# Optimization experiments

Hardware: AMD Instinct MI355X
Metric: run time of the kernel (lower is better)

Reference implementation:

```python
import jax, jax.numpy as jnp
import numpy as np

B, NQ, NK = 16, 1024, 1024
DQ = DK = DV = 512
H = 4
DH = DV // H  # 128


def layer_norm(x, g, b, eps=1e-5):
    mu = jnp.mean(x, axis=-1, keepdims=True)
    var = jnp.var(x, axis=-1, keepdims=True)  # biased, matches torch LayerNorm
    return (x - mu) / jnp.sqrt(var + eps) * g + b


def setup_inputs() -> dict:
    key = jax.random.key(0)
    ks = jax.random.split(key, 16)
    s = lambda d: 1.0 / np.sqrt(d)
    return {
        "Q": jax.random.normal(ks[0], (B, NQ, DQ), jnp.float32),
        "K": jax.random.normal(ks[1], (B, NK, DK), jnp.float32),
        "weights": jax.random.uniform(ks[2], (H * B, NQ, NK), jnp.float32),
        "Wq": jax.random.normal(ks[3], (DV, DQ), jnp.float32) * s(DQ),
        "bq": jnp.zeros((DV,), jnp.float32),
        "Wk": jax.random.normal(ks[4], (DV, DK), jnp.float32) * s(DK),
        "bk": jnp.zeros((DV,), jnp.float32),
        "Wv": jax.random.normal(ks[5], (DV, DK), jnp.float32) * s(DK),
        "bv": jnp.zeros((DV,), jnp.float32),
        "Wo": jax.random.normal(ks[6], (DV, DV), jnp.float32) * s(DV),
        "bo": jnp.zeros((DV,), jnp.float32),
        "g0": jnp.ones((DV,), jnp.float32),
        "beta0": jnp.zeros((DV,), jnp.float32),
        "g1": jnp.ones((DV,), jnp.float32),
        "beta1": jnp.zeros((DV,), jnp.float32),
    }


def reference(Q, K, weights, Wq, bq, Wk, bk, Wv, bv, Wo, bo, g0, beta0, g1, beta1):
    q = Q @ Wq.T + bq  # [B,NQ,DV]
    k = K @ Wk.T + bk  # [B,NK,DV]
    v = K @ Wv.T + bv  # [B,NK,DV]

    # torch split(dh, 2) + cat(0) == head-major [H,B,N,DH]
    def heads(x, n):
        return x.reshape(B, n, H, DH).transpose(2, 0, 1, 3)

    q_, k_, v_ = heads(q, NQ), heads(k, NK), heads(v, NK)

    # NOTE: original scales by sqrt(dim_V), not sqrt(head_dim)
    scores = jnp.einsum("hbqd,hbkd->hbqk", q_, k_) / np.sqrt(DV)
    log_w = jnp.log(jnp.clip(weights, 0.0, None)).reshape(H, B, NQ, NK)
    A = jax.nn.softmax(scores + log_w, axis=-1)  # [H,B,NQ,NK]

    o = q_ + jnp.einsum("hbqk,hbkd->hbqd", A, v_)  # residual inside heads
    # split(B,0)+cat(2) == merge heads back to [B,NQ,DV]
    O = o.transpose(1, 2, 0, 3).reshape(B, NQ, DV)
    O = layer_norm(O, g0, beta0)
    O = O + jax.nn.relu(O @ Wo.T + bo)
    O = layer_norm(O, g1, beta1)
    return O
```

## Files before the change

kernel.cpp:

```cpp
#include <hip/hip_runtime.h>

typedef unsigned short u16;
typedef unsigned int u32;
typedef __attribute__((ext_vector_type(8))) short short8;
typedef __attribute__((ext_vector_type(4))) float f32x4;
typedef __attribute__((ext_vector_type(2))) u32 uintx2;
typedef __attribute__((address_space(3))) u32 lds32;
typedef const __attribute__((address_space(1))) u32 g32c;

__device__ __forceinline__ u16 f2bf(float f) {
  union { float f; u32 u; } v; v.f = f;
  return (u16)((v.u + 0x7fffu + ((v.u >> 16) & 1u)) >> 16);
}
__device__ __forceinline__ float bf2f(u16 h) {
  union { u32 u; float f; } v; v.u = ((u32)h) << 16;
  return v.f;
}

__global__ void cvt_w_kernel(const float* __restrict__ Wq, const float* __restrict__ Wk,
                             const float* __restrict__ Wv, const float* __restrict__ Wo,
                             u16* __restrict__ dst) {
  int m = blockIdx.y;
  const float* s = (m == 0) ? Wq : (m == 1) ? Wk : (m == 2) ? Wv : Wo;
  int idx = (blockIdx.x * 256 + threadIdx.x) * 4;
  float4 v = *(const float4*)(s + idx);
  uintx2 pk;
  pk[0] = (u32)f2bf(v.x) | ((u32)f2bf(v.y) << 16);
  pk[1] = (u32)f2bf(v.z) | ((u32)f2bf(v.w) << 16);
  *(uintx2*)(dst + m * 262144 + idx) = pk;
}

template <bool AF32, bool OUTMODE, bool TRANSV>
__device__ __forceinline__ void gemm_bt_body(const void* __restrict__ Ap,
                                             const u16* __restrict__ Bw,
                                             const float* __restrict__ bias,
                                             u16* __restrict__ C) {
  __shared__ u16 ldsA[128 * 64];
  __shared__ u16 ldsB[128 * 64];
  const int t = threadIdx.x;
  const int lane = t & 63, wid = t >> 6;
  const int lr = lane & 15, lg = lane >> 4;
  const int n0 = blockIdx.x * 128;
  const int m0 = blockIdx.y * 128;
  const int wr = (wid >> 1) * 64, wc = (wid & 1) * 64;

  f32x4 acc[4][4];
#pragma unroll
  for (int i = 0; i < 4; ++i)
#pragma unroll
    for (int j = 0; j < 4; ++j)
#pragma unroll
      for (int r = 0; r < 4; ++r) acc[i][j][r] = 0.f;

  for (int kt = 0; kt < 512; kt += 64) {
    __syncthreads();
#pragma unroll
    for (int i = 0; i < 4; ++i) {
      int lin = i * 256 + t;
      int row = lin >> 3, u = lin & 7;
      int pu = u ^ (row & 7);
      if constexpr (AF32) {
        const float* src = (const float*)Ap + (size_t)(m0 + row) * 512 + kt + u * 8;
        float4 v0 = *(const float4*)src;
        float4 v1 = *(const float4*)(src + 4);
        short8 pk;
        pk[0] = (short)f2bf(v0.x); pk[1] = (short)f2bf(v0.y);
        pk[2] = (short)f2bf(v0.z); pk[3] = (short)f2bf(v0.w);
        pk[4] = (short)f2bf(v1.x); pk[5] = (short)f2bf(v1.y);
        pk[6] = (short)f2bf(v1.z); pk[7] = (short)f2bf(v1.w);
        *(short8*)&ldsA[row * 64 + pu * 8] = pk;
      } else {
        const u16* src = (const u16*)Ap + (size_t)(m0 + row) * 512 + kt + u * 8;
        *(short8*)&ldsA[row * 64 + pu * 8] = *(const short8*)src;
      }
      const u16* bsrc = Bw + (size_t)(n0 + row) * 512 + kt + u * 8;
      *(short8*)&ldsB[row * 64 + pu * 8] = *(const short8*)bsrc;
    }
    __syncthreads();
#pragma unroll
    for (int kk = 0; kk < 2; ++kk) {
      short8 af[4], bfr[4];
#pragma unroll
      for (int mf = 0; mf < 4; ++mf) {
        int row = wr + mf * 16 + lr;
        af[mf] = *(const short8*)&ldsA[row * 64 + (((kk * 4 + lg) ^ (row & 7)) * 8)];
      }
#pragma unroll
      for (int nf = 0; nf < 4; ++nf) {
        int row = wc + nf * 16 + lr;
        bfr[nf] = *(const short8*)&ldsB[row * 64 + (((kk * 4 + lg) ^ (row & 7)) * 8)];
      }
#pragma unroll
      for (int mf = 0; mf < 4; ++mf)
#pragma unroll
        for (int nf = 0; nf < 4; ++nf)
          acc[mf][nf] =
              __builtin_amdgcn_mfma_f32_16x16x32_bf16(af[mf], bfr[nf], acc[mf][nf], 0, 0, 0);
    }
  }

  if constexpr (TRANSV) {
    const int h_ = n0 >> 7;
#pragma unroll
    for (int mf = 0; mf < 4; ++mf)
#pragma unroll
      for (int nf = 0; nf < 4; ++nf) {
        int d = wc + nf * 16 + lr;
        int rr0 = m0 + wr + mf * 16 + lg * 4;
        int b_ = rr0 >> 10;
        int k0 = rr0 & 1023;
        float bvv = bias[n0 + d];
        uintx2 pk;
        pk[0] = (u32)f2bf(acc[mf][nf][0] + bvv) | ((u32)f2bf(acc[mf][nf][1] + bvv) << 16);
        pk[1] = (u32)f2bf(acc[mf][nf][2] + bvv) | ((u32)f2bf(acc[mf][nf][3] + bvv) << 16);
        *(uintx2*)(C + (((size_t)b_ * 4 + h_) * 128 + d) * 1024 + k0) = pk;
      }
  } else {
#pragma unroll
    for (int mf = 0; mf < 4; ++mf)
#pragma unroll
      for (int nf = 0; nf < 4; ++nf) {
        int c = n0 + wc + nf * 16 + lr;
        float bv = bias[c];
#pragma unroll
        for (int r = 0; r < 4; ++r) {
          int rr = m0 + wr + mf * 16 + lg * 4 + r;
          float v = acc[mf][nf][r] + bv;
          if constexpr (OUTMODE) {
            v = v > 0.f ? v : 0.f;
            v += bf2f(((const u16*)Ap)[(size_t)rr * 512 + c]);
          }
          C[(size_t)rr * 512 + c] = f2bf(v);
        }
      }
  }
}

__global__ __launch_bounds__(256) void gemm3_kernel(const float* __restrict__ Q,
                                                    const float* __restrict__ K,
                                                    const u16* __restrict__ Wb,
                                                    const float* __restrict__ bq,
                                                    const float* __restrict__ bk,
                                                    const float* __restrict__ bv,
                                                    u16* qb, u16* kb, u16* vbT) {
  int z = blockIdx.z;
  if (z == 2) {
    gemm_bt_body<true, false, true>(K, Wb + 524288, bv, vbT);
  } else {
    const void* Ap = (z == 0) ? (const void*)Q : (const void*)K;
    const u16* Bw = Wb + z * 262144;
    const float* bias = (z == 0) ? bq : bk;
    u16* C = (z == 0) ? qb : kb;
    gemm_bt_body<true, false, false>(Ap, Bw, bias, C);
  }
}

__global__ __launch_bounds__(256) void gemmo_kernel(const u16* __restrict__ X,
                                                    const u16* __restrict__ Wb,
                                                    const float* __restrict__ bo,
                                                    u16* Z) {
  gemm_bt_body<false, true, false>(X, Wb, bo, Z);
}

__global__ __launch_bounds__(256) void attn_kernel(const u16* __restrict__ qb,
                                                   const u16* __restrict__ kb,
                                                   const u16* __restrict__ vbT,
                                                   const float* __restrict__ Wt,
                                                   u16* __restrict__ Ob) {
  __shared__ __align__(16) u16 ldsK[2][64 * 128];
  __shared__ __align__(16) u16 ldsVT[2][128 * 64];
  __shared__ __align__(16) u16 ldsP[128 * 64];
  const int t = threadIdx.x;
  const int lane = t & 63, wid = t >> 6;
  const int lr = lane & 15, lg = lane >> 4;
  const int bid = blockIdx.x;
  const int x_ = bid & 7, s_ = bid >> 3;
  const int hb = ((s_ & 7) << 3) | x_;
  const int q0 = (s_ >> 3) * 128;
  const int b = hb & 15;
  const int h = hb >> 4;
  const int wq = wid * 32;
  const size_t kvbase = ((size_t)b * 1024) * 512 + h * 128;
  const size_t vtbase = ((size_t)b * 4 + h) * 131072;
  const float SCALE = 0.044194173824159216f;

  const u16* ksrc[4];
  const u16* vtsrc[4];
#pragma unroll
  for (int i = 0; i < 4; ++i) {
    {
      int lin = i * 256 + t;
      int row = lin >> 4, u = lin & 15;
      ksrc[i] = kb + kvbase + (size_t)row * 512 + ((u ^ (row & 15)) * 8);
    }
    {
      int lin = i * 256 + t;
      int row = lin >> 3, u = lin & 7;
      vtsrc[i] = vbT + vtbase + (size_t)row * 1024 + ((u ^ (row & 7)) * 8);
    }
  }
  const int wslot = (t & 192) * 8;

#define STAGE(bu)                                                                           \
  do {                                                                                      \
    _Pragma("unroll") for (int i_ = 0; i_ < 4; ++i_) {                                      \
      __builtin_amdgcn_global_load_lds((g32c*)(ksrc[i_]),                                   \
                                       (lds32*)(&ldsK[bu][i_ * 2048 + wslot]), 16, 0, 0);   \
      __builtin_amdgcn_global_load_lds((g32c*)(vtsrc[i_]),                                  \
                                       (lds32*)(&ldsVT[bu][i_ * 2048 + wslot]), 16, 0, 0);  \
      ksrc[i_] += 32768;                                                \
      vtsrc[i_] += 64;                                                  \
    }                                                                                       \
  } while (0)

  const float* wp0 = Wt + ((size_t)hb * 1024 + q0 + wq + lr) * 1024 + lg * 4;
  const float* wp1 = wp0 + 16 * 1024;

#define WLOADP(W)                                          \
  do {                                                     \
    _Pragma("unroll") for (int j_ = 0; j_ < 4; ++j_) {     \
      W[j_]     = *(const f32x4*)(wp0 + j_ * 16);          \
      W[4 + j_] = *(const f32x4*)(wp1 + j_ * 16);          \
    }                                                      \
    wp0 += 64; wp1 += 64;                                  \
  } while (0)

  short8 qfr[2][4];
#pragma unroll
  for (int nf = 0; nf < 2; ++nf) {
    const u16* qp = qb + kvbase + (size_t)(q0 + wq + nf * 16 + lr) * 512 + lg * 8;
#pragma unroll
    for (int ds = 0; ds < 4; ++ds) qfr[nf][ds] = *(const short8*)(qp + ds * 32);
  }

  f32x4 oacc[2][8];
#pragma unroll
  for (int i = 0; i < 2; ++i)
#pragma unroll
    for (int j = 0; j < 8; ++j)
#pragma unroll
      for (int r = 0; r < 4; ++r) oacc[i][j][r] = 0.f;
  float lacc[2] = {0.f, 0.f};

  auto tile_compute = [&](const u16* bK, const u16* bVT, const f32x4 (&W)[8]) {
    f32x4 sacc[4][2];
#pragma unroll
    for (int i = 0; i < 4; ++i)
#pragma unroll
      for (int j = 0; j < 2; ++j)
#pragma unroll
        for (int r = 0; r < 4; ++r) sacc[i][j][r] = 0.f;

#pragma unroll
    for (int ds = 0; ds < 4; ++ds) {
      short8 kf[4];
#pragma unroll
      for (int mf = 0; mf < 4; ++mf) {
        int row = mf * 16 + lr;
        kf[mf] = *(const short8*)&bK[row * 128 + (((ds * 4 + lg) ^ (row & 15)) * 8)];
      }
      __builtin_amdgcn_s_setprio(1);
#pragma unroll
      for (int mf = 0; mf < 4; ++mf)
#pragma unroll
        for (int nf = 0; nf < 2; ++nf)
          sacc[mf][nf] =
              __builtin_amdgcn_mfma_f32_16x16x32_bf16(kf[mf], qfr[nf][ds], sacc[mf][nf], 0, 0, 0);
      __builtin_amdgcn_s_setprio(0);
    }

#pragma unroll
    for (int nf = 0; nf < 2; ++nf) {
      int prow = wq + nf * 16 + lr;
#pragma unroll
      for (int mf = 0; mf < 4; ++mf) {
        f32x4 w4 = W[nf * 4 + mf];
        float p0 = w4[0] * __expf(sacc[mf][nf][0] * SCALE);
        float p1 = w4[1] * __expf(sacc[mf][nf][1] * SCALE);
        float p2 = w4[2] * __expf(sacc[mf][nf][2] * SCALE);
        float p3 = w4[3] * __expf(sacc[mf][nf][3] * SCALE);
        lacc[nf] += (p0 + p1) + (p2 + p3);
        uintx2 pk;
        pk[0] = (u32)f2bf(p0) | ((u32)f2bf(p1) << 16);
        pk[1] = (u32)f2bf(p2) | ((u32)f2bf(p3) << 16);
        int byteoff = (prow * 128 + (mf * 16 + lg * 4) * 2) ^ ((prow & 7) << 4);
        *(uintx2*)((char*)ldsP + byteoff) = pk;
      }
    }

#pragma unroll
    for (int ks = 0; ks < 2; ++ks) {
      short8 pa[2];
#pragma unroll
      for (int qf = 0; qf < 2; ++qf) {
        int row = wq + qf * 16 + lr;
        int byteoff = (row * 128 + (ks * 4 + lg) * 16) ^ ((row & 7) << 4);
        pa[qf] = *(const short8*)((const char*)ldsP + byteoff);
      }
      short8 vf[8];
#pragma unroll
      for (int nf = 0; nf < 8; ++nf) {
        int row = nf * 16 + lr;
        vf[nf] = *(const short8*)&bVT[row * 64 + (((ks * 4 + lg) ^ (row & 7)) * 8)];
      }
      __builtin_amdgcn_s_setprio(1);
#pragma unroll
      for (int qf = 0; qf < 2; ++qf)
#pragma unroll
        for (int nf = 0; nf < 8; ++nf)
          oacc[qf][nf] =
              __builtin_amdgcn_mfma_f32_16x16x32_bf16(pa[qf], vf[nf], oacc[qf][nf], 0, 0, 0);
      __builtin_amdgcn_s_setprio(0);
    }
  };

#define SCHED_FENCE() __builtin_amdgcn_sched_barrier(0)
#define WAITBAR(N)                                                 \
  do {                                                             \
    SCHED_FENCE();                                                 \
    asm volatile("s_waitcnt vmcnt(" #N ")" ::: "memory");          \
    __builtin_amdgcn_s_barrier();                                  \
    SCHED_FENCE();                                                 \
  } while (0)
#define BAR()                                                      \
  do {                                                             \
    SCHED_FENCE();                                                 \
    __builtin_amdgcn_s_barrier();                                  \
    SCHED_FENCE();                                                 \
  } while (0)

  f32x4 wA[8], wB[8];
  WLOADP(wA);
  STAGE(0);

  for (int it = 0; it < 8; ++it) {
    {
      STAGE(1);
      WLOADP(wB);
      WAITBAR(16);
      tile_compute(&ldsK[0][0], &ldsVT[0][0], wA);
      BAR();
    }
    {
      if (it < 7) {
        STAGE(0);
        WLOADP(wA);
        WAITBAR(16);
      } else {
        WAITBAR(0);
      }
      tile_compute(&ldsK[1][0], &ldsVT[1][0], wB);
      if (it < 7) BAR();
    }
  }

  float lred[2];
#pragma unroll
  for (int nf = 0; nf < 2; ++nf) {
    float s = lacc[nf];
    s += __shfl_xor(s, 16);
    s += __shfl_xor(s, 32);
    lred[nf] = s;
  }

#pragma unroll
  for (int qf = 0; qf < 2; ++qf)
#pragma unroll
    for (int r = 0; r < 4; ++r) {
      float lv = __shfl(lred[qf], (lane & 48) | (lg * 4 + r));
      float linv = 1.0f / lv;
      int qrow = q0 + wq + qf * 16 + lg * 4 + r;
      size_t base = kvbase + (size_t)qrow * 512;
#pragma unroll
      for (int nf = 0; nf < 8; ++nf) {
        size_t idx = base + nf * 16 + lr;
        Ob[idx] = f2bf(bf2f(qb[idx]) + oacc[qf][nf][r] * linv);
      }
    }
#undef STAGE
#undef WLOADP
#undef WAITBAR
#undef BAR
#undef SCHED_FENCE
}

template <bool F32OUT>
__global__ __launch_bounds__(256) void ln_kernel(const u16* __restrict__ in,
                                                 const float* __restrict__ g,
                                                 const float* __restrict__ be,
                                                 void* __restrict__ outp) {
  const int lane = threadIdx.x & 63, wid = threadIdx.x >> 6;
  const int row = blockIdx.x * 4 + wid;
  const u16* p = in + (size_t)row * 512 + lane * 8;
  short8 v = *(const short8*)p;
  float x[8];
  float s = 0.f, s2 = 0.f;
#pragma unroll
  for (int j = 0; j < 8; ++j) {
    x[j] = bf2f((u16)v[j]);
    s += x[j];
    s2 += x[j] * x[j];
  }
#pragma unroll
  for (int off = 1; off < 64; off <<= 1) {
    s += __shfl_xor(s, off);
    s2 += __shfl_xor(s2, off);
  }
  float mu = s * (1.f / 512.f);
  float var = s2 * (1.f / 512.f) - mu * mu;
  float rs = rsqrtf(var + 1e-5f);
  float4 ga = *(const float4*)(g + lane * 8);
  float4 gb = *(const float4*)(g + lane * 8 + 4);
  float4 ba = *(const float4*)(be + lane * 8);
  float4 bb = *(const float4*)(be + lane * 8 + 4);
  float gg[8] = {ga.x, ga.y, ga.z, ga.w, gb.x, gb.y, gb.z, gb.w};
  float bv[8] = {ba.x, ba.y, ba.z, ba.w, bb.x, bb.y, bb.z, bb.w};
  if constexpr (F32OUT) {
    float* out = (float*)outp + (size_t)row * 512 + lane * 8;
    float4 o0, o1;
    o0.x = (x[0] - mu) * rs * gg[0] + bv[0];
    o0.y = (x[1] - mu) * rs * gg[1] + bv[1];
    o0.z = (x[2] - mu) * rs * gg[2] + bv[2];
    o0.w = (x[3] - mu) * rs * gg[3] + bv[3];
    o1.x = (x[4] - mu) * rs * gg[4] + bv[4];
    o1.y = (x[5] - mu) * rs * gg[5] + bv[5];
    o1.z = (x[6] - mu) * rs * gg[6] + bv[6];
    o1.w = (x[7] - mu) * rs * gg[7] + bv[7];
    *(float4*)out = o0;
    *(float4*)(out + 4) = o1;
  } else {
    short8 o;
#pragma unroll
    for (int j = 0; j < 8; ++j) o[j] = (short)f2bf((x[j] - mu) * rs * gg[j] + bv[j]);
    *(short8*)((u16*)outp + (size_t)row * 512 + lane * 8) = o;
  }
}

extern "C" void kernel_launch(void* const* d_in, const int* in_sizes, int n_in,
                              void* d_out, int out_size, void* d_ws, size_t ws_size,
                              hipStream_t stream) {
  (void)in_sizes; (void)n_in; (void)out_size; (void)ws_size;
  const float* Q   = (const float*)d_in[0];
  const float* K   = (const float*)d_in[1];
  const float* Wt  = (const float*)d_in[2];
  const float* Wq  = (const float*)d_in[3];
  const float* bq  = (const float*)d_in[4];
  const float* Wk  = (const float*)d_in[5];
  const float* bk  = (const float*)d_in[6];
  const float* Wv  = (const float*)d_in[7];
  const float* bv  = (const float*)d_in[8];
  const float* Wo  = (const float*)d_in[9];
  const float* bo  = (const float*)d_in[10];
  const float* g0  = (const float*)d_in[11];
  const float* be0 = (const float*)d_in[12];
  const float* g1  = (const float*)d_in[13];
  const float* be1 = (const float*)d_in[14];

  char* ws = (char*)d_ws;
  const size_t MB16 = 16777216;
  u16* qb  = (u16*)(ws);
  u16* kb  = (u16*)(ws + MB16);
  u16* vbT = (u16*)(ws + 2 * MB16);
  u16* Wb  = (u16*)(ws + 3 * MB16);
  u16* Ob  = (u16*)d_out;

  cvt_w_kernel<<<dim3(256, 4), 256, 0, stream>>>(Wq, Wk, Wv, Wo, Wb);
  gemm3_kernel<<<dim3(4, 128, 3), 256, 0, stream>>>(Q, K, Wb, bq, bk, bv, qb, kb, vbT);
  attn_kernel<<<dim3(512), 256, 0, stream>>>(qb, kb, vbT, Wt, Ob);
  ln_kernel<false><<<4096, 256, 0, stream>>>(Ob, g0, be0, qb);
  gemmo_kernel<<<dim3(4, 128), 256, 0, stream>>>(qb, Wb + 786432, bo, kb);
  ln_kernel<true><<<4096, 256, 0, stream>>>(kb, g1, be1, d_out);
}
```

Baseline: 251.9 us.

## Double-buffer projection GEMMs with async global-to-LDS loads and register prefetch

Rewrites the QKV projection and output GEMMs to use double-buffered LDS tiles. The weight (and bf16 activation) tiles are loaded with direct global-to-LDS loads, and the fp32 A operand is prefetched two stages ahead in registers before conversion to bf16. This overlaps global memory latency with the MFMA work and needs one barrier per k-step instead of two. The cost is double the LDS footprint and more registers, which may lower occupancy.

```diff
diff --git a/kernel.cpp b/kernel.cpp
--- a/kernel.cpp
+++ b/kernel.cpp
@@ -30,19 +30,58 @@
   *(uintx2*)(dst + m * 262144 + idx) = pk;
 }
 
-template <bool AF32, bool OUTMODE, bool TRANSV>
-__device__ __forceinline__ void gemm_bt_body(const void* __restrict__ Ap,
-                                             const u16* __restrict__ Bw,
-                                             const float* __restrict__ bias,
-                                             u16* __restrict__ C) {
-  __shared__ u16 ldsA[128 * 64];
-  __shared__ u16 ldsB[128 * 64];
+
+__device__ __forceinline__ void gemm_tile_mfma(const u16* bA, const u16* bB, int wr, int wc,
+                                               int lr, int lg, f32x4 (&acc)[4][4]) {
+#pragma unroll
+  for (int kk = 0; kk < 2; ++kk) {
+    short8 af[4], bfr[4];
+#pragma unroll
+    for (int mf = 0; mf < 4; ++mf) {
+      int row = wr + mf * 16 + lr;
+      af[mf] = *(const short8*)&bA[row * 64 + (((kk * 4 + lg) ^ (row & 7)) * 8)];
+    }
+#pragma unroll
+    for (int nf = 0; nf < 4; ++nf) {
+      int row = wc + nf * 16 + lr;
+      bfr[nf] = *(const short8*)&bB[row * 64 + (((kk * 4 + lg) ^ (row & 7)) * 8)];
+    }
+#pragma unroll
+    for (int mf = 0; mf < 4; ++mf)
+#pragma unroll
+      for (int nf = 0; nf < 4; ++nf)
+        acc[mf][nf] =
+            __builtin_amdgcn_mfma_f32_16x16x32_bf16(af[mf], bfr[nf], acc[mf][nf], 0, 0, 0);
+  }
+}
+
+template <bool TRANSV>
+__device__ __forceinline__ void gemm_f32a_body(const float* __restrict__ Ap,
+                                               const u16* __restrict__ Bw,
+                                               const float* __restrict__ bias,
+                                               u16* __restrict__ C) {
+  __shared__ __align__(16) u16 ldsA[2][128 * 64];
+  __shared__ __align__(16) u16 ldsB[2][128 * 64];
   const int t = threadIdx.x;
   const int lane = t & 63, wid = t >> 6;
   const int lr = lane & 15, lg = lane >> 4;
   const int n0 = blockIdx.x * 128;
   const int m0 = blockIdx.y * 128;
   const int wr = (wid >> 1) * 64, wc = (wid & 1) * 64;
+  const int wslot = (t & 192) * 8;
+
+  int arow[4], apu[4];
+  const u16* bsrc[4];
+  const float* asrc[4];
+#pragma unroll
+  for (int i = 0; i < 4; ++i) {
+    int lin = i * 256 + t;
+    int row = lin >> 3, u = lin & 7;
+    arow[i] = row;
+    apu[i] = u ^ (row & 7);
+    asrc[i] = Ap + (size_t)(m0 + row) * 512 + u * 8;
+    bsrc[i] = Bw + (size_t)(n0 + row) * 512 + ((u ^ (row & 7)) * 8);
+  }
 
   f32x4 acc[4][4];
 #pragma unroll
@@ -52,52 +91,61 @@
 #pragma unroll
       for (int r = 0; r < 4; ++r) acc[i][j][r] = 0.f;
 
-  for (int kt = 0; kt < 512; kt += 64) {
-    __syncthreads();
-#pragma unroll
-    for (int i = 0; i < 4; ++i) {
-      int lin = i * 256 + t;
-      int row = lin >> 3, u = lin & 7;
-      int pu = u ^ (row & 7);
-      if constexpr (AF32) {
-        const float* src = (const float*)Ap + (size_t)(m0 + row) * 512 + kt + u * 8;
-        float4 v0 = *(const float4*)src;
-        float4 v1 = *(const float4*)(src + 4);
-        short8 pk;
-        pk[0] = (short)f2bf(v0.x); pk[1] = (short)f2bf(v0.y);
-        pk[2] = (short)f2bf(v0.z); pk[3] = (short)f2bf(v0.w);
-        pk[4] = (short)f2bf(v1.x); pk[5] = (short)f2bf(v1.y);
-        pk[6] = (short)f2bf(v1.z); pk[7] = (short)f2bf(v1.w);
-        *(short8*)&ldsA[row * 64 + pu * 8] = pk;
-      } else {
-        const u16* src = (const u16*)Ap + (size_t)(m0 + row) * 512 + kt + u * 8;
-        *(short8*)&ldsA[row * 64 + pu * 8] = *(const short8*)src;
-      }
-      const u16* bsrc = Bw + (size_t)(n0 + row) * 512 + kt + u * 8;
-      *(short8*)&ldsB[row * 64 + pu * 8] = *(const short8*)bsrc;
-    }
-    __syncthreads();
-#pragma unroll
-    for (int kk = 0; kk < 2; ++kk) {
-      short8 af[4], bfr[4];
-#pragma unroll
-      for (int mf = 0; mf < 4; ++mf) {
-        int row = wr + mf * 16 + lr;
-        af[mf] = *(const short8*)&ldsA[row * 64 + (((kk * 4 + lg) ^ (row & 7)) * 8)];
-      }
-#pragma unroll
-      for (int nf = 0; nf < 4; ++nf) {
-        int row = wc + nf * 16 + lr;
-        bfr[nf] = *(const short8*)&ldsB[row * 64 + (((kk * 4 + lg) ^ (row & 7)) * 8)];
-      }
-#pragma unroll
-      for (int mf = 0; mf < 4; ++mf)
-#pragma unroll
-        for (int nf = 0; nf < 4; ++nf)
-          acc[mf][nf] =
-              __builtin_amdgcn_mfma_f32_16x16x32_bf16(af[mf], bfr[nf], acc[mf][nf], 0, 0, 0);
-    }
-  }
+  float4 rA[2][8];
+
+#define BISSUE(bu, kt)                                                                      \
+  do {                                                                                      \
+    _Pragma("unroll") for (int i_ = 0; i_ < 4; ++i_) {                                      \
+      __builtin_amdgcn_global_load_lds((g32c*)(bsrc[i_] + (kt)),                            \
+                                       (lds32*)(&ldsB[bu][i_ * 2048 + wslot]), 16, 0, 0);   \
+    }                                                                                       \
+  } while (0)
+#define AISSUE(set, kt)                                                                     \
+  do {                                                                                      \
+    _Pragma("unroll") for (int i_ = 0; i_ < 4; ++i_) {                                      \
+      rA[set][2 * i_] = *(const float4*)(asrc[i_] + (kt));                                  \
+      rA[set][2 * i_ + 1] = *(const float4*)(asrc[i_] + (kt) + 4);                          \
+    }                                                                                       \
+  } while (0)
+#define AWRITE(set, bu)                                                                     \
+  do {                                                                                      \
+    _Pragma("unroll") for (int i_ = 0; i_ < 4; ++i_) {                                      \
+      float4 v0 = rA[set][2 * i_], v1 = rA[set][2 * i_ + 1];                                \
+      short8 pk;                                                                            \
+      pk[0] = (short)f2bf(v0.x); pk[1] = (short)f2bf(v0.y);                                 \
+      pk[2] = (short)f2bf(v0.z); pk[3] = (short)f2bf(v0.w);                                 \
+      pk[4] = (short)f2bf(v1.x); pk[5] = (short)f2bf(v1.y);                                 \
+      pk[6] = (short)f2bf(v1.z); pk[7] = (short)f2bf(v1.w);                                 \
+      *(short8*)&ldsA[bu][arow[i_] * 64 + apu[i_] * 8] = pk;                                \
+    }                                                                                       \
+  } while (0)
+#define DRAINBAR()                                                     \
+  do {                                                                 \
+    asm volatile("s_waitcnt vmcnt(0) lgkmcnt(0)" ::: "memory");        \
+    __builtin_amdgcn_s_barrier();                                      \
+  } while (0)
+
+  BISSUE(0, 0);
+  AISSUE(0, 0);
+  AWRITE(0, 0);
+  AISSUE(1, 64);
+  DRAINBAR();
+
+#pragma unroll
+  for (int p = 0; p < 8; ++p) {
+    const int buf = p & 1, nbuf = buf ^ 1;
+    if (p < 7) {
+      BISSUE(nbuf, (p + 1) * 64);
+      AWRITE((p + 1) & 1, nbuf);
+      if (p < 6) AISSUE(p & 1, (p + 2) * 64);
+    }
+    gemm_tile_mfma(&ldsA[buf][0], &ldsB[buf][0], wr, wc, lr, lg, acc);
+    if (p < 7) DRAINBAR();
+  }
+#undef BISSUE
+#undef AISSUE
+#undef AWRITE
+#undef DRAINBAR
 
   if constexpr (TRANSV) {
     const int h_ = n0 >> 7;
@@ -125,12 +173,7 @@
 #pragma unroll
         for (int r = 0; r < 4; ++r) {
           int rr = m0 + wr + mf * 16 + lg * 4 + r;
-          float v = acc[mf][nf][r] + bv;
-          if constexpr (OUTMODE) {
-            v = v > 0.f ? v : 0.f;
-            v += bf2f(((const u16*)Ap)[(size_t)rr * 512 + c]);
-          }
-          C[(size_t)rr * 512 + c] = f2bf(v);
+          C[(size_t)rr * 512 + c] = f2bf(acc[mf][nf][r] + bv);
         }
       }
   }
@@ -145,21 +188,88 @@
                                                     u16* qb, u16* kb, u16* vbT) {
   int z = blockIdx.z;
   if (z == 2) {
-    gemm_bt_body<true, false, true>(K, Wb + 524288, bv, vbT);
+    gemm_f32a_body<true>(K, Wb + 524288, bv, vbT);
+  } else if (z == 1) {
+    gemm_f32a_body<false>(K, Wb + 262144, bk, kb);
   } else {
-    const void* Ap = (z == 0) ? (const void*)Q : (const void*)K;
-    const u16* Bw = Wb + z * 262144;
-    const float* bias = (z == 0) ? bq : bk;
-    u16* C = (z == 0) ? qb : kb;
-    gemm_bt_body<true, false, false>(Ap, Bw, bias, C);
+    gemm_f32a_body<false>(Q, Wb, bq, qb);
   }
 }
 
 __global__ __launch_bounds__(256) void gemmo_kernel(const u16* __restrict__ X,
                                                     const u16* __restrict__ Wb,
                                                     const float* __restrict__ bo,
-                                                    u16* Z) {
-  gemm_bt_body<false, true, false>(X, Wb, bo, Z);
+                                                    u16* __restrict__ Z) {
+  __shared__ __align__(16) u16 ldsA[2][128 * 64];
+  __shared__ __align__(16) u16 ldsB[2][128 * 64];
+  const int t = threadIdx.x;
+  const int lane = t & 63, wid = t >> 6;
+  const int lr = lane & 15, lg = lane >> 4;
+  const int n0 = blockIdx.x * 128;
+  const int m0 = blockIdx.y * 128;
+  const int wr = (wid >> 1) * 64, wc = (wid & 1) * 64;
+  const int wslot = (t & 192) * 8;
+
+  const u16* asrc[4];
+  const u16* bsrc[4];
+#pragma unroll
+  for (int i = 0; i < 4; ++i) {
+    int lin = i * 256 + t;
+    int row = lin >> 3, u = lin & 7;
+    int pu = (u ^ (row & 7)) * 8;
+    asrc[i] = X + (size_t)(m0 + row) * 512 + pu;
+    bsrc[i] = Wb + (size_t)(n0 + row) * 512 + pu;
+  }
+
+  f32x4 acc[4][4];
+#pragma unroll
+  for (int i = 0; i < 4; ++i)
+#pragma unroll
+    for (int j = 0; j < 4; ++j)
+#pragma unroll
+      for (int r = 0; r < 4; ++r) acc[i][j][r] = 0.f;
+
+#define STAGEO(bu, kt)                                                                      \
+  do {                                                                                      \
+    _Pragma("unroll") for (int i_ = 0; i_ < 4; ++i_) {                                      \
+      __builtin_amdgcn_global_load_lds((g32c*)(asrc[i_] + (kt)),                            \
+                                       (lds32*)(&ldsA[bu][i_ * 2048 + wslot]), 16, 0, 0);   \
+      __builtin_amdgcn_global_load_lds((g32c*)(bsrc[i_] + (kt)),                            \
+                                       (lds32*)(&ldsB[bu][i_ * 2048 + wslot]), 16, 0, 0);   \
+    }                                                                                       \
+  } while (0)
+
+  STAGEO(0, 0);
+  asm volatile("s_waitcnt vmcnt(0)" ::: "memory");
+  __builtin_amdgcn_s_barrier();
+
+#pragma unroll
+  for (int p = 0; p < 8; ++p) {
+    const int buf = p & 1, nbuf = buf ^ 1;
+    if (p < 7) STAGEO(nbuf, (p + 1) * 64);
+    gemm_tile_mfma(&ldsA[buf][0], &ldsB[buf][0], wr, wc, lr, lg, acc);
+    if (p < 7) {
+      asm volatile("s_waitcnt vmcnt(0)" ::: "memory");
+      __builtin_amdgcn_s_barrier();
+    }
+  }
+#undef STAGEO
+
+#pragma unroll
+  for (int mf = 0; mf < 4; ++mf)
+#pragma unroll
+    for (int nf = 0; nf < 4; ++nf) {
+      int c = n0 + wc + nf * 16 + lr;
+      float bv = bo[c];
+#pragma unroll
+      for (int r = 0; r < 4; ++r) {
+        int rr = m0 + wr + mf * 16 + lg * 4 + r;
+        float v = acc[mf][nf][r] + bv;
+        v = v > 0.f ? v : 0.f;
+        v += bf2f(X[(size_t)rr * 512 + c]);
+        Z[(size_t)rr * 512 + c] = f2bf(v);
+      }
+    }
 }
 
 __global__ __launch_bounds__(256) void attn_kernel(const u16* __restrict__ qb,
@@ -208,8 +318,8 @@
                                        (lds32*)(&ldsK[bu][i_ * 2048 + wslot]), 16, 0, 0);   \
       __builtin_amdgcn_global_load_lds((g32c*)(vtsrc[i_]),                                  \
                                        (lds32*)(&ldsVT[bu][i_ * 2048 + wslot]), 16, 0, 0);  \
-      ksrc[i_] += 32768;                                                \
-      vtsrc[i_] += 64;                                                  \
+      ksrc[i_] += 32768;                                                                    \
+      vtsrc[i_] += 64;                                                                      \
     }                                                                                       \
   } while (0)
 
```

Result: slower. 268.0 us (+6.4%).
